# Kernel tuning notes

Measured on AMD Instinct MI355X. Metric: run time of the kernel, lower is better.

The kernel has to match this reference:

```python
import jax, jax.numpy as jnp
import numpy as np

N_EMBED = 1024
N_HEAD = 16
SEQ = 2048
BATCH = 2


def setup_inputs() -> dict:
    key = jax.random.key(0)
    ks = jax.random.split(key, 5)
    scale_in = 1.0 / np.sqrt(N_EMBED)
    x = jax.random.normal(ks[0], (BATCH, SEQ, N_EMBED), dtype=jnp.float32)
    # attn_proj: Linear(n_embed, 3*n_embed); stored as [in, out] so y = x @ W + b
    W_qkv = jax.random.normal(ks[1], (N_EMBED, 3 * N_EMBED), dtype=jnp.float32) * scale_in
    b_qkv = jax.random.normal(ks[2], (3 * N_EMBED,), dtype=jnp.float32) * 0.01
    # fin_proj: Linear(n_embed, n_embed)
    W_out = jax.random.normal(ks[3], (N_EMBED, N_EMBED), dtype=jnp.float32) * scale_in
    b_out = jax.random.normal(ks[4], (N_EMBED,), dtype=jnp.float32) * 0.01
    return {"x": x, "W_qkv": W_qkv, "b_qkv": b_qkv, "W_out": W_out, "b_out": b_out}


def reference(x, W_qkv, b_qkv, W_out, b_out):
    B, S, D = x.shape
    H = N_HEAD
    hd = D // H
    qkv = x @ W_qkv + b_qkv  # [B, S, 3D]
    q, k, v = jnp.split(qkv, 3, axis=-1)
    # [B, H, S, hd]
    q = q.reshape(B, S, H, hd).transpose(0, 2, 1, 3)
    k = k.reshape(B, S, H, hd).transpose(0, 2, 1, 3)
    v = v.reshape(B, S, H, hd).transpose(0, 2, 1, 3)
    scores = jnp.einsum("bhqd,bhkd->bhqk", q, k) * (1.0 / np.sqrt(hd))
    causal = jnp.tril(jnp.ones((S, S), dtype=bool))  # lower-triangular mask
    scores = jnp.where(causal[None, None], scores, -jnp.inf)
    probs = jax.nn.softmax(scores, axis=-1)
    # dropout is identity in eval mode (inference reference)
    attn = jnp.einsum("bhqk,bhkd->bhqd", probs, v)  # [B, H, S, hd]
    attn = attn.transpose(0, 2, 1, 3).reshape(B, S, D)
    return attn @ W_out + b_out
```

## Files before the change

kernel.cpp:

```cpp
#include <hip/hip_runtime.h>

typedef short bf16x8 __attribute__((ext_vector_type(8)));
typedef short bf16x4 __attribute__((ext_vector_type(4)));
typedef float f32x4 __attribute__((ext_vector_type(4)));
typedef int i32x4 __attribute__((ext_vector_type(4)));
typedef int i32x2 __attribute__((ext_vector_type(2)));

#define MFMA16x16x32(a, b, c) __builtin_amdgcn_mfma_f32_16x16x32_bf16(a, b, c, 0, 0, 0)
#define TRR(dst, a) asm volatile("ds_read_b64_tr_b16 %0, %1" : "=v"(dst) : "v"(a))

__device__ __forceinline__ unsigned short f2bf(float f) {
  union { float f; unsigned u; } v; v.f = f;
  unsigned u = v.u + 0x7FFFu + ((v.u >> 16) & 1u);
  return (unsigned short)(u >> 16);
}

__device__ __forceinline__ unsigned cvtpk(float lo, float hi) {
  unsigned r;
  asm("v_cvt_pk_bf16_f32 %0, %1, %2" : "=v"(r) : "v"(lo), "v"(hi));
  return r;
}

__device__ __forceinline__ float max3f(float a, float b, float c) {
  float d;
  asm("v_max3_f32 %0, %1, %2, %3" : "=v"(d) : "v"(a), "v"(b), "v"(c));
  return d;
}

__device__ __forceinline__ void gload16(const void* g, void* l) {
  __builtin_amdgcn_global_load_lds((const __attribute__((address_space(1))) void*)g,
                                   (__attribute__((address_space(3))) void*)l, 16, 0, 0);
}

__device__ __forceinline__ unsigned ldsoff(const void* p) {
  return (unsigned)(unsigned long long)(const __attribute__((address_space(3))) void*)p;
}

__global__ __launch_bounds__(256) void prep(const float* __restrict__ x,
                                            unsigned short* __restrict__ xb,
                                            const float* __restrict__ Wq,
                                            unsigned short* __restrict__ WqT,
                                            const float* __restrict__ Wo,
                                            unsigned short* __restrict__ WoT,
                                            int* __restrict__ ctr) {
  __shared__ float tile[32][33];
  int bid = blockIdx.x;
  int t = threadIdx.x;
  if (bid == 0 && t < 32) ctr[t * 16] = 0;
  if (bid < 2048) {
    long i = (long)bid * 256 + t;
    const float4* p = reinterpret_cast<const float4*>(x + i * 8);
    float4 a = p[0], b = p[1];
    i32x4 o;
    o[0] = cvtpk(a.x, a.y); o[1] = cvtpk(a.z, a.w);
    o[2] = cvtpk(b.x, b.y); o[3] = cvtpk(b.z, b.w);
    *reinterpret_cast<i32x4*>(xb + i * 8) = o;
    return;
  }
  const float* W; unsigned short* Wt; int N, bx, by;
  if (bid < 5120) {
    W = Wq; Wt = WqT; N = 3072;
    int r = bid - 2048; bx = r % 96; by = r / 96;
  } else {
    W = Wo; Wt = WoT; N = 1024;
    int r = bid - 5120; bx = r & 31; by = r >> 5;
  }
  const int K = 1024;
  int tx = t & 31, ty = t >> 5;
  int n0 = bx << 5, k0 = by << 5;
#pragma unroll
  for (int i = 0; i < 32; i += 8)
    tile[ty + i][tx] = W[(long)(k0 + ty + i) * N + n0 + tx];
  __syncthreads();
#pragma unroll
  for (int i = 0; i < 32; i += 8)
    Wt[(long)(n0 + ty + i) * K + k0 + tx] = f2bf(tile[tx][ty + i]);
}

template <int BF16OUT>
__global__ __launch_bounds__(256) void gemm_bt(const unsigned short* __restrict__ A,
                                               const unsigned short* __restrict__ Bt,
                                               const float* __restrict__ bias,
                                               void* __restrict__ Cv,
                                               int M, int N, int K) {
  __shared__ __align__(128) unsigned short As[3][4096];
  __shared__ __align__(128) unsigned short Bs[3][4096];
  int t = threadIdx.x;
  int w = t >> 6, l = t & 63;
  int g = l >> 4, m16 = l & 15;
  int wr = w >> 1, wc = w & 1;
  int nwg = gridDim.x * gridDim.y;
  int f = blockIdx.y * gridDim.x + blockIdx.x;
  int q8 = nwg >> 3;
  int s = (f & 7) * q8 + (f >> 3);
  int bx = s % gridDim.x, by = s / gridDim.x;
  long am0 = (long)by << 7;
  long bn0 = (long)bx << 7;

  int seg0 = w, seg1 = 4 + w;
  int fl0 = (seg0 << 9) + (l << 3), fl1 = (seg1 << 9) + (l << 3);
  int r0 = fl0 >> 5, c0 = fl0 & 31;
  int r1 = fl1 >> 5, c1 = fl1 & 31;

  f32x4 acc[4][4];
#pragma unroll
  for (int i = 0; i < 4; ++i)
#pragma unroll
    for (int j = 0; j < 4; ++j) acc[i][j] = (f32x4){0.f, 0.f, 0.f, 0.f};

  gload16(A + (am0 + r0) * K + c0, &As[0][seg0 << 9]);
  gload16(A + (am0 + r1) * K + c1, &As[0][seg1 << 9]);
  gload16(Bt + (bn0 + r0) * K + c0, &Bs[0][seg0 << 9]);
  gload16(Bt + (bn0 + r1) * K + c1, &Bs[0][seg1 << 9]);
  gload16(A + (am0 + r0) * K + 32 + c0, &As[1][seg0 << 9]);
  gload16(A + (am0 + r1) * K + 32 + c1, &As[1][seg1 << 9]);
  gload16(Bt + (bn0 + r0) * K + 32 + c0, &Bs[1][seg0 << 9]);
  gload16(Bt + (bn0 + r1) * K + 32 + c1, &Bs[1][seg1 << 9]);

  int cur = 0;
  for (int k0 = 0; k0 < K; k0 += 32) {
    if (k0 + 32 < K)
      asm volatile("s_waitcnt vmcnt(4)" ::: "memory");
    else
      asm volatile("s_waitcnt vmcnt(0)" ::: "memory");
    __syncthreads();
    if (k0 + 64 < K) {
      int kn = k0 + 64;
      int nb = cur + 2; if (nb >= 3) nb -= 3;
      gload16(A + (am0 + r0) * K + kn + c0, &As[nb][seg0 << 9]);
      gload16(A + (am0 + r1) * K + kn + c1, &As[nb][seg1 << 9]);
      gload16(Bt + (bn0 + r0) * K + kn + c0, &Bs[nb][seg0 << 9]);
      gload16(Bt + (bn0 + r1) * K + kn + c1, &Bs[nb][seg1 << 9]);
    }
    bf16x8 af[4], bfr[4];
#pragma unroll
    for (int im = 0; im < 4; ++im)
      af[im] = *(const bf16x8*)&As[cur][((wr << 6) + (im << 4) + m16) * 32 + (g << 3)];
#pragma unroll
    for (int in = 0; in < 4; ++in)
      bfr[in] = *(const bf16x8*)&Bs[cur][((wc << 6) + (in << 4) + m16) * 32 + (g << 3)];
    __builtin_amdgcn_s_setprio(1);
#pragma unroll
    for (int im = 0; im < 4; ++im)
#pragma unroll
      for (int in = 0; in < 4; ++in)
        acc[im][in] = MFMA16x16x32(af[im], bfr[in], acc[im][in]);
    __builtin_amdgcn_s_setprio(0);
    cur = cur == 2 ? 0 : cur + 1;
  }

#pragma unroll
  for (int im = 0; im < 4; ++im) {
#pragma unroll
    for (int in = 0; in < 4; ++in) {
      long col = bn0 + (wc << 6) + (in << 4) + m16;
      float bval = bias[col];
#pragma unroll
      for (int r = 0; r < 4; ++r) {
        long row = am0 + (wr << 6) + (im << 4) + (g << 2) + r;
        float v = acc[im][in][r] + bval;
        if (BF16OUT)
          ((unsigned short*)Cv)[row * N + col] = f2bf(v);
        else
          ((float*)Cv)[row * N + col] = v;
      }
    }
  }
}

__global__ __launch_bounds__(256, 3) void attn_fwd(const unsigned short* __restrict__ qkv,
                                                   unsigned short* __restrict__ out,
                                                   int* __restrict__ ctr) {
  const int D3 = 3072;
  const float C1 = 0.18033688f;
  const float THR = 11.5415603f;
  __shared__ __align__(128) unsigned short Ks[2][4096];
  __shared__ __align__(128) unsigned short Vs[2][4096];
  __shared__ int s_idx;
  int bh = blockIdx.x;
  int b = bh >> 4, h = bh & 15;
  int* myctr = ctr + bh * 16;
  int t = threadIdx.x;
  int w = t >> 6, l = t & 63;
  int g = l >> 4, m16 = l & 15;
  long base = (long)b * 2048 * D3;
  const unsigned short* kbase = qkv + base + 1024 + h * 64;
  const unsigned short* vbase = qkv + base + 2048 + h * 64;

  int l8 = l >> 3, sc = l & 7;
  int kof = (w * 8 + l8) * D3 + ((sc ^ l8) << 3);
  int s0 = w * 8 + l8;
  int vof = ((s0 & 15) * 4 + (sc >> 1)) * D3 + ((s0 >> 4) << 4) + ((sc & 1) << 3);
  const f32x4 zero4 = (f32x4){0.f, 0.f, 0.f, 0.f};

  for (;;) {
    if (t == 0) s_idx = atomicAdd(myctr, 1);
    __syncthreads();
    int idx = s_idx;
    if (idx >= 32) return;
    int qt = 31 - idx;

    int qrow = (qt << 6) + (w << 4) + m16;
    const unsigned short* qp = qkv + base + (long)qrow * D3 + h * 64;
    bf16x8 qf0 = *(const bf16x8*)(qp + g * 8);
    bf16x8 qf1 = *(const bf16x8*)(qp + 32 + g * 8);

    f32x4 O[4];
#pragma unroll
    for (int d = 0; d < 4; ++d) O[d] = zero4;
    f32x4 lsv = zero4;
    float m2 = -1e30f;
    int nt = qt + 1;

    gload16(kbase + kof, &Ks[0][w << 9]);
    gload16(kbase + 32 * D3 + kof, &Ks[0][2048 + (w << 9)]);
    gload16(vbase + vof, &Vs[0][w << 9]);
    gload16(vbase + vof + 32, &Vs[0][2048 + (w << 9)]);

    int buf = 0;
    for (int ss = 0; ss < nt; ++ss) {
      asm volatile("s_waitcnt vmcnt(0)" ::: "memory");
      __syncthreads();
      if (ss + 1 < nt) {
        long off = (long)(ss + 1) * 64 * D3;
        gload16(kbase + off + kof, &Ks[buf ^ 1][w << 9]);
        gload16(kbase + off + 32 * D3 + kof, &Ks[buf ^ 1][2048 + (w << 9)]);
        gload16(vbase + off + vof, &Vs[buf ^ 1][w << 9]);
        gload16(vbase + off + vof + 32, &Vs[buf ^ 1][2048 + (w << 9)]);
      }

      unsigned va = ldsoff(&Vs[buf][0]) + (g << 7) + (m16 << 3);
      bf16x4 t0[4], t1[4], t2[4], t3[4];
#pragma unroll
      for (int d = 0; d < 4; ++d) {
        unsigned a = va + (d << 11);
        TRR(t0[d], a);
        TRR(t1[d], a + 512);
        TRR(t2[d], a + 1024);
        TRR(t3[d], a + 1536);
      }
      const char* kbuf = (const char*)&Ks[buf][0];
      int swz = m16 & 7;
      f32x4 st[4];
      __builtin_amdgcn_s_setprio(1);
#pragma unroll
      for (int T = 0; T < 4; ++T) {
        const char* rp = kbuf + (((T << 4) + m16) << 7);
        bf16x8 kf0 = *(const bf16x8*)(rp + ((g ^ swz) << 4));
        bf16x8 kf1 = *(const bf16x8*)(rp + (((4 + g) ^ swz) << 4));
        st[T] = MFMA16x16x32(kf0, qf0, zero4);
        st[T] = MFMA16x16x32(kf1, qf1, st[T]);
      }
      __builtin_amdgcn_s_setprio(0);

      if (ss == nt - 1) {
        int rq = qrow - (ss << 6);
#pragma unroll
        for (int T = 0; T < 4; ++T)
#pragma unroll
          for (int r = 0; r < 4; ++r)
            if ((T << 4) + (g << 2) + r > rq) st[T][r] = -3e38f;
      }
      float tm[4];
#pragma unroll
      for (int T = 0; T < 4; ++T)
        tm[T] = max3f(fmaxf(st[T][0], st[T][1]), st[T][2], st[T][3]);
      float tmax = fmaxf(max3f(tm[0], tm[1], tm[2]), tm[3]);
      tmax = fmaxf(tmax, __shfl_xor(tmax, 16));
      tmax = fmaxf(tmax, __shfl_xor(tmax, 32));
      float tsc2 = tmax * C1;
      bool skip = __all(tsc2 <= m2 + THR);
      float mnew2 = skip ? m2 : fmaxf(m2, tsc2);
      float p[4][4];
      f32x4 ts4 = zero4;
#pragma unroll
      for (int T = 0; T < 4; ++T)
#pragma unroll
        for (int r = 0; r < 4; ++r) {
          float e = __builtin_amdgcn_exp2f(fmaf(st[T][r], C1, -mnew2));
          p[T][r] = e;
          ts4[r] += e;
        }
      if (!skip) {
        float alpha = __builtin_amdgcn_exp2f(m2 - mnew2);
        lsv *= alpha;
#pragma unroll
        for (int d = 0; d < 4; ++d) O[d] *= alpha;
        m2 = mnew2;
      }
      lsv += ts4;

      i32x4 w0, w1;
      w0[0] = cvtpk(p[0][0], p[0][1]); w0[1] = cvtpk(p[0][2], p[0][3]);
      w0[2] = cvtpk(p[1][0], p[1][1]); w0[3] = cvtpk(p[1][2], p[1][3]);
      w1[0] = cvtpk(p[2][0], p[2][1]); w1[1] = cvtpk(p[2][2], p[2][3]);
      w1[2] = cvtpk(p[3][0], p[3][1]); w1[3] = cvtpk(p[3][2], p[3][3]);
      bf16x8 pb0 = __builtin_bit_cast(bf16x8, w0);
      bf16x8 pb1 = __builtin_bit_cast(bf16x8, w1);

      asm volatile("s_waitcnt lgkmcnt(0)" ::: "memory");
      __builtin_amdgcn_sched_barrier(0);

      bf16x8 vfA[4], vfB[4];
#pragma unroll
      for (int d = 0; d < 4; ++d) {
        vfA[d] = __builtin_shufflevector(t0[d], t1[d], 0, 1, 2, 3, 4, 5, 6, 7);
        vfB[d] = __builtin_shufflevector(t2[d], t3[d], 0, 1, 2, 3, 4, 5, 6, 7);
      }
      __builtin_amdgcn_s_setprio(1);
#pragma unroll
      for (int d = 0; d < 4; ++d) {
        O[d] = MFMA16x16x32(vfA[d], pb0, O[d]);
        O[d] = MFMA16x16x32(vfB[d], pb1, O[d]);
      }
      __builtin_amdgcn_s_setprio(0);
      buf ^= 1;
    }

    float s = (lsv[0] + lsv[1]) + (lsv[2] + lsv[3]);
    s += __shfl_xor(s, 16);
    s += __shfl_xor(s, 32);
    float inv = 1.0f / s;
    unsigned short* op = out + (long)(b * 2048 + qrow) * 1024 + h * 64;
#pragma unroll
    for (int d = 0; d < 4; ++d) {
      i32x2 pk;
      pk[0] = (int)cvtpk(O[d][0] * inv, O[d][1] * inv);
      pk[1] = (int)cvtpk(O[d][2] * inv, O[d][3] * inv);
      *reinterpret_cast<i32x2*>(op + (d << 4) + (g << 2)) = pk;
    }
  }
}

extern "C" void kernel_launch(void* const* d_in, const int* in_sizes, int n_in,
                              void* d_out, int out_size, void* d_ws, size_t ws_size,
                              hipStream_t stream) {
  const float* x     = (const float*)d_in[0];
  const float* W_qkv = (const float*)d_in[1];
  const float* b_qkv = (const float*)d_in[2];
  const float* W_out = (const float*)d_in[3];
  const float* b_out = (const float*)d_in[4];

  char* ws = (char*)d_ws;
  int* ctr = (int*)ws;
  unsigned short* xb    = (unsigned short*)(ws + 4096);
  unsigned short* wqkvT = (unsigned short*)(ws + 4096 + (8l << 20));
  unsigned short* woutT = (unsigned short*)(ws + 4096 + (14l << 20));
  unsigned short* qkv   = (unsigned short*)(ws + 4096 + (16l << 20));

  prep<<<6144, 256, 0, stream>>>(x, xb, W_qkv, wqkvT, W_out, woutT, ctr);
  gemm_bt<1><<<dim3(24, 32), 256, 0, stream>>>(xb, wqkvT, b_qkv, (void*)qkv, 4096, 3072, 1024);
  attn_fwd<<<dim3(32, 24), 256, 0, stream>>>(qkv, xb, ctr);
  gemm_bt<0><<<dim3(8, 32), 256, 0, stream>>>(xb, woutT, b_out, d_out, 4096, 1024, 1024);
}
```

Measured before the change: 107.1 us.

## Split long causal attention query tiles across two workers and merge partials

Query tiles 16-31 now have their KV range split into two halves, each processed as a separate work item. The partial O, max and sum are written in fp32 to workspace, and a new merge kernel combines them with log-sum-exp weighting. A static work-item table orders items longest first. Occupancy is raised to 4 blocks per CU, and the grid grows to 32 blocks per head. The aim is to shorten the critical path from the longest causal tiles and improve load balance, at the cost of extra partial-result traffic and one more kernel launch.

```diff
diff --git a/kernel.cpp b/kernel.cpp
--- a/kernel.cpp
+++ b/kernel.cpp
@@ -35,6 +35,19 @@
 __device__ __forceinline__ unsigned ldsoff(const void* p) {
   return (unsigned)(unsigned long long)(const __attribute__((address_space(3))) void*)p;
 }
+
+__device__ const unsigned char g_items[48] = {
+  (31<<2)|2|0, (31<<2)|2|1, (30<<2)|2|0, (15<<2),
+  (30<<2)|2|1, (29<<2)|2|0, (29<<2)|2|1, (28<<2)|2|0, (14<<2),
+  (28<<2)|2|1, (27<<2)|2|0, (27<<2)|2|1, (26<<2)|2|0, (13<<2),
+  (26<<2)|2|1, (25<<2)|2|0, (25<<2)|2|1, (24<<2)|2|0, (12<<2),
+  (24<<2)|2|1, (23<<2)|2|0, (23<<2)|2|1, (22<<2)|2|0, (11<<2),
+  (22<<2)|2|1, (21<<2)|2|0, (21<<2)|2|1, (20<<2)|2|0, (10<<2),
+  (20<<2)|2|1, (19<<2)|2|0, (19<<2)|2|1, (18<<2)|2|0, (9<<2),
+  (18<<2)|2|1, (17<<2)|2|0, (17<<2)|2|1, (16<<2)|2|0, (8<<2),
+  (16<<2)|2|1, (7<<2),
+  (6<<2), (5<<2), (4<<2), (3<<2), (2<<2), (1<<2), (0<<2)
+};
 
 __global__ __launch_bounds__(256) void prep(const float* __restrict__ x,
                                             unsigned short* __restrict__ xb,
@@ -168,9 +181,11 @@
   }
 }
 
-__global__ __launch_bounds__(256, 3) void attn_fwd(const unsigned short* __restrict__ qkv,
+__global__ __launch_bounds__(256, 4) void attn_fwd(const unsigned short* __restrict__ qkv,
                                                    unsigned short* __restrict__ out,
-                                                   int* __restrict__ ctr) {
+                                                   int* __restrict__ ctr,
+                                                   float* __restrict__ pO,
+                                                   float* __restrict__ pML) {
   const int D3 = 3072;
   const float C1 = 0.18033688f;
   const float THR = 11.5415603f;
@@ -197,8 +212,14 @@
     if (t == 0) s_idx = atomicAdd(myctr, 1);
     __syncthreads();
     int idx = s_idx;
-    if (idx >= 32) return;
-    int qt = 31 - idx;
+    if (idx >= 48) return;
+    unsigned e = g_items[idx];
+    int qt = e >> 2;
+    int split = (e >> 1) & 1, half = e & 1;
+    int ntf = qt + 1;
+    int h0 = (ntf + 1) >> 1;
+    int ss0 = (split && half) ? h0 : 0;
+    int ssEnd = split ? (half ? ntf : h0) : ntf;
 
     int qrow = (qt << 6) + (w << 4) + m16;
     const unsigned short* qp = qkv + base + (long)qrow * D3 + h * 64;
@@ -210,18 +231,20 @@
     for (int d = 0; d < 4; ++d) O[d] = zero4;
     f32x4 lsv = zero4;
     float m2 = -1e30f;
-    int nt = qt + 1;
-
-    gload16(kbase + kof, &Ks[0][w << 9]);
-    gload16(kbase + 32 * D3 + kof, &Ks[0][2048 + (w << 9)]);
-    gload16(vbase + vof, &Vs[0][w << 9]);
-    gload16(vbase + vof + 32, &Vs[0][2048 + (w << 9)]);
+
+    {
+      long off = (long)ss0 * 64 * D3;
+      gload16(kbase + off + kof, &Ks[0][w << 9]);
+      gload16(kbase + off + 32 * D3 + kof, &Ks[0][2048 + (w << 9)]);
+      gload16(vbase + off + vof, &Vs[0][w << 9]);
+      gload16(vbase + off + vof + 32, &Vs[0][2048 + (w << 9)]);
+    }
 
     int buf = 0;
-    for (int ss = 0; ss < nt; ++ss) {
+    for (int ss = ss0; ss < ssEnd; ++ss) {
       asm volatile("s_waitcnt vmcnt(0)" ::: "memory");
       __syncthreads();
-      if (ss + 1 < nt) {
+      if (ss + 1 < ssEnd) {
         long off = (long)(ss + 1) * 64 * D3;
         gload16(kbase + off + kof, &Ks[buf ^ 1][w << 9]);
         gload16(kbase + off + 32 * D3 + kof, &Ks[buf ^ 1][2048 + (w << 9)]);
@@ -253,7 +276,7 @@
       }
       __builtin_amdgcn_s_setprio(0);
 
-      if (ss == nt - 1) {
+      if (ss == qt) {
         int rq = qrow - (ss << 6);
 #pragma unroll
         for (int T = 0; T < 4; ++T)
@@ -277,9 +300,9 @@
       for (int T = 0; T < 4; ++T)
 #pragma unroll
         for (int r = 0; r < 4; ++r) {
-          float e = __builtin_amdgcn_exp2f(fmaf(st[T][r], C1, -mnew2));
-          p[T][r] = e;
-          ts4[r] += e;
+          float e2 = __builtin_amdgcn_exp2f(fmaf(st[T][r], C1, -mnew2));
+          p[T][r] = e2;
+          ts4[r] += e2;
         }
       if (!skip) {
         float alpha = __builtin_amdgcn_exp2f(m2 - mnew2);
@@ -320,15 +343,61 @@
     float s = (lsv[0] + lsv[1]) + (lsv[2] + lsv[3]);
     s += __shfl_xor(s, 16);
     s += __shfl_xor(s, 32);
-    float inv = 1.0f / s;
-    unsigned short* op = out + (long)(b * 2048 + qrow) * 1024 + h * 64;
-#pragma unroll
-    for (int d = 0; d < 4; ++d) {
-      i32x2 pk;
-      pk[0] = (int)cvtpk(O[d][0] * inv, O[d][1] * inv);
-      pk[1] = (int)cvtpk(O[d][2] * inv, O[d][3] * inv);
-      *reinterpret_cast<i32x2*>(op + (d << 4) + (g << 2)) = pk;
+    if (split) {
+      int row = (w << 4) + m16;
+      long pbase = (long)((bh << 4) + (qt - 16)) * 2 + half;
+      float* po = pO + (pbase << 12) + row * 64;
+#pragma unroll
+      for (int d = 0; d < 4; ++d)
+        *reinterpret_cast<f32x4*>(po + (d << 4) + (g << 2)) = O[d];
+      if (g == 0) {
+        float* pm = pML + (pbase << 7) + row * 2;
+        pm[0] = m2;
+        pm[1] = s;
+      }
+    } else {
+      float inv = 1.0f / s;
+      unsigned short* op = out + (long)(b * 2048 + qrow) * 1024 + h * 64;
+#pragma unroll
+      for (int d = 0; d < 4; ++d) {
+        i32x2 pk;
+        pk[0] = (int)cvtpk(O[d][0] * inv, O[d][1] * inv);
+        pk[1] = (int)cvtpk(O[d][2] * inv, O[d][3] * inv);
+        *reinterpret_cast<i32x2*>(op + (d << 4) + (g << 2)) = pk;
+      }
     }
+  }
+}
+
+__global__ __launch_bounds__(256) void attn_merge(const float* __restrict__ pO,
+                                                  const float* __restrict__ pML,
+                                                  unsigned short* __restrict__ out) {
+  int blk = blockIdx.x;
+  int bh = blk >> 4, qtIdx = blk & 15;
+  int qt = 16 + qtIdx;
+  int b = bh >> 4, h = bh & 15;
+  int t = threadIdx.x;
+  int row = t >> 2, cq = (t & 3) << 4;
+  long pbase = (long)blk * 2;
+  const float* o0 = pO + (pbase << 12) + row * 64 + cq;
+  const float* o1 = o0 + 4096;
+  const float* ml0 = pML + (pbase << 7) + row * 2;
+  const float* ml1 = ml0 + 128;
+  float m0 = ml0[0], l0 = ml0[1];
+  float m1 = ml1[0], l1 = ml1[1];
+  float M = fmaxf(m0, m1);
+  float w0 = exp2f(m0 - M), w1 = exp2f(m1 - M);
+  float inv = 1.0f / (l0 * w0 + l1 * w1);
+  w0 *= inv; w1 *= inv;
+  unsigned short* op = out + ((long)(b * 2048 + qt * 64 + row)) * 1024 + h * 64 + cq;
+#pragma unroll
+  for (int i = 0; i < 4; ++i) {
+    float4 a = *reinterpret_cast<const float4*>(o0 + i * 4);
+    float4 c = *reinterpret_cast<const float4*>(o1 + i * 4);
+    i32x2 pk;
+    pk[0] = (int)cvtpk(a.x * w0 + c.x * w1, a.y * w0 + c.y * w1);
+    pk[1] = (int)cvtpk(a.z * w0 + c.z * w1, a.w * w0 + c.w * w1);
+    *reinterpret_cast<i32x2*>(op + i * 4) = pk;
   }
 }
 
@@ -347,9 +416,12 @@
   unsigned short* wqkvT = (unsigned short*)(ws + 4096 + (8l << 20));
   unsigned short* woutT = (unsigned short*)(ws + 4096 + (14l << 20));
   unsigned short* qkv   = (unsigned short*)(ws + 4096 + (16l << 20));
+  float* pO  = (float*)(ws + 4096 + (40l << 20));
+  float* pML = (float*)(ws + 4096 + (56l << 20));
 
   prep<<<6144, 256, 0, stream>>>(x, xb, W_qkv, wqkvT, W_out, woutT, ctr);
   gemm_bt<1><<<dim3(24, 32), 256, 0, stream>>>(xb, wqkvT, b_qkv, (void*)qkv, 4096, 3072, 1024);
-  attn_fwd<<<dim3(32, 24), 256, 0, stream>>>(qkv, xb, ctr);
+  attn_fwd<<<dim3(32, 32), 256, 0, stream>>>(qkv, xb, ctr, pO, pML);
+  attn_merge<<<512, 256, 0, stream>>>(pO, pML, xb);
   gemm_bt<0><<<dim3(8, 32), 256, 0, stream>>>(xb, woutT, b_out, d_out, 4096, 1024, 1024);
 }
```

New measurement: 110.1 us. 1.03x slower.
